# Optimization experiments

Measured on AMD Instinct MI355X. Metric: run time of the kernel, lower is better.

The kernel has to match this reference:

```python
import jax, jax.numpy as jnp
import numpy as np

H = 512      # hidden_dim
K = 3        # conv_kernel_size
CHUNK = 3    # chunk_size
EPS = 1e-5   # BatchNorm eps


def conv1d(x, w, b, pad):
    # x: (B, Cin, L), w: (Cout, Cin, K)
    y = jax.lax.conv_general_dilated(x, w, (1,), [(pad, pad)],
                                     dimension_numbers=("NCH", "OIH", "NCH"))
    return y + b[None, :, None]


def chunk_indices(seq_lens):
    # static int metadata -> numpy index build (loop over small fixed batch only)
    sl = np.asarray(seq_lens)
    bidx, sidx = [], []
    for b, l in enumerate(sl):
        starts = np.arange(0, int(l) - CHUNK + 1, CHUNK)
        bidx.append(np.full(starts.shape[0], b, dtype=np.int32))
        sidx.append(starts.astype(np.int32))
    return np.concatenate(bidx), np.concatenate(sidx)


def setup_inputs() -> dict:
    key = jax.random.key(0)
    ks = jax.random.split(key, 8)
    B, L = 32, 4096
    x = jax.random.normal(ks[0], (B, L), jnp.float32)
    seq_lens = jax.random.randint(ks[1], (B,), 2048, L + 1)

    def w(k, shape):
        return jax.random.normal(k, shape, jnp.float32) * 0.05

    return {
        "x": x,
        "w0": w(ks[2], (H, 1, K)), "b0": jnp.zeros((H,)), "g0": jnp.ones((H,)), "be0": jnp.zeros((H,)),
        "w1": w(ks[3], (H, H, K)), "b1": jnp.zeros((H,)), "g1": jnp.ones((H,)), "be1": jnp.zeros((H,)),
        "w2": w(ks[4], (H, H, K)), "b2": jnp.zeros((H,)), "g2": jnp.ones((H,)), "be2": jnp.zeros((H,)),
        "pw": w(ks[5], (H, H, CHUNK)), "pb": jnp.zeros((H,)),
        "fw": w(ks[6], (1, H)), "fb": jnp.zeros((1,)),
        "seq_lens": seq_lens,
    }


def reference(x, w0, b0, g0, be0, w1, b1, g1, be1, w2, b2, g2, be2,
              pw, pb, fw, fb, seq_lens):
    inv = np.float32(1.0 / np.sqrt(1.0 + EPS))  # BN eval: mean=0, var=1
    h = x[:, None, :]  # (B, 1, L)
    for (w, b, g, be) in ((w0, b0, g0, be0), (w1, b1, g1, be1), (w2, b2, g2, be2)):
        h = jax.nn.relu(conv1d(h, w, b, pad=1))
        h = (g * inv)[None, :, None] * h + be[None, :, None]
    h = jnp.transpose(h, (0, 2, 1))  # (B, L, H)

    bidx_np, sidx_np = chunk_indices(seq_lens)
    bidx = jnp.asarray(bidx_np)
    sidx = jnp.asarray(sidx_np)
    offs = jnp.arange(CHUNK, dtype=jnp.int32)
    chunks = h[bidx[:, None], sidx[:, None] + offs[None, :], :]  # (N, CHUNK, H)

    # pre_fc_conv over a length-CHUNK window == one GEMM per chunk
    z = jnp.einsum("nth,cht->nc", chunks, pw) + pb  # (N, H)
    logits = jax.nn.relu(z) @ fw.T + fb             # (N, 1)
    return jax.nn.sigmoid(logits)[:, 0]             # (N,)
```

## Files before the change

### kernel.cpp

```cpp
#include <hip/hip_runtime.h>

#define HCH 512
#define LSEQ 4096
#define NB 32
#define KW 3
#define KDIM 1536
#define SPAD 1408
#define INVS 0.9999950000374997f

typedef __attribute__((ext_vector_type(8))) short bf16x8;
typedef __attribute__((ext_vector_type(4))) float f32x4;

__device__ inline unsigned short f2bf(float f) {
  unsigned int u = __float_as_uint(f);
  u += 0x7fffu + ((u >> 16) & 1u);
  return (unsigned short)(u >> 16);
}

__device__ inline void gl_lds16(const void* g, void* l) {
  __builtin_amdgcn_global_load_lds(
      (const __attribute__((address_space(1))) void*)g,
      (__attribute__((address_space(3))) void*)l, 16, 0, 0);
}

__global__ void prepz(const int* __restrict__ seq_lens, int* __restrict__ cum,
                      float* __restrict__ p, int n) {
  int i = blockIdx.x * 256 + threadIdx.x;
  if (i < n) p[i] = 0.f;
  if (blockIdx.x == 0 && threadIdx.x == 0) {
    int acc = 0;
    for (int b = 0; b < NB; b++) {
      cum[b] = acc;
      acc += (seq_lens[b] - KW) / KW + 1;
    }
  }
}

__global__ void wtrans(const float* __restrict__ w1, const float* __restrict__ w2,
                       const float* __restrict__ pw, unsigned short* __restrict__ wt) {
  int idx = blockIdx.x * 256 + threadIdx.x;
  int which = idx / (HCH * KDIM);
  int r = idx % (HCH * KDIM);
  int c = r / KDIM;
  int rem = r % KDIM;
  int k = rem / HCH, ci = rem % HCH;
  const float* src = (which == 0) ? w1 : ((which == 1) ? w2 : pw);
  wt[idx] = f2bf(src[c * KDIM + ci * KW + k]);
}

__global__ void layer0(const float* __restrict__ x, const float* __restrict__ w0,
                       const float* __restrict__ b0, const float* __restrict__ g0,
                       const float* __restrict__ be0, unsigned short* __restrict__ h0) {
  int tid = threadIdx.x;
  int wave = tid >> 6, lane = tid & 63;
  int pos0 = (blockIdx.x * 4 + wave) * 8;
  int l0 = pos0 & (LSEQ - 1);
  int c0 = lane * 8;

  float w[24], bb[8], gg[8], ee[8];
  for (int v = 0; v < 6; v++)
    *reinterpret_cast<float4*>(w + v * 4) = *reinterpret_cast<const float4*>(w0 + c0 * 3 + v * 4);
  for (int v = 0; v < 2; v++) {
    *reinterpret_cast<float4*>(bb + v * 4) = *reinterpret_cast<const float4*>(b0 + c0 + v * 4);
    *reinterpret_cast<float4*>(gg + v * 4) = *reinterpret_cast<const float4*>(g0 + c0 + v * 4);
    *reinterpret_cast<float4*>(ee + v * 4) = *reinterpret_cast<const float4*>(be0 + c0 + v * 4);
  }
  for (int c = 0; c < 8; c++) gg[c] *= INVS;

  const float* xb = x + (size_t)(pos0 - l0);
  for (int pp = 0; pp < 8; pp++) {
    int l = l0 + pp;
    float xm1 = (l > 0) ? xb[l - 1] : 0.f;
    float xc = xb[l];
    float xp1 = (l < LSEQ - 1) ? xb[l + 1] : 0.f;
    unsigned int o[4];
    for (int pq = 0; pq < 4; pq++) {
      unsigned int lo = 0, hi = 0;
      for (int s = 0; s < 2; s++) {
        int c = pq * 2 + s;
        float y = w[c * 3] * xm1 + w[c * 3 + 1] * xc + w[c * 3 + 2] * xp1 + bb[c];
        y = fmaxf(y, 0.f);
        unsigned int u = f2bf(gg[c] * y + ee[c]);
        if (s == 0) lo = u; else hi = u;
      }
      o[pq] = lo | (hi << 16);
    }
    uint4 v4; v4.x = o[0]; v4.y = o[1]; v4.z = o[2]; v4.w = o[3];
    *reinterpret_cast<uint4*>(h0 + (size_t)(pos0 + pp) * HCH + c0) = v4;
  }
}

__global__ __launch_bounds__(256, 2) void conv_gemm(
    const unsigned short* __restrict__ hin,
    const unsigned short* __restrict__ wT,
    const float* __restrict__ bconv, const float* __restrict__ g,
    const float* __restrict__ be,
    unsigned short* __restrict__ hout,
    const unsigned short* __restrict__ zp) {
  __shared__ unsigned short As[3 * 128 * 32];
  __shared__ unsigned short Bs[272 * 32];

  int tid = threadIdx.x;
  int wave = tid >> 6, lane = tid & 63;
  int cm = blockIdx.x * 128;
  int ntile = blockIdx.y;
  int b = ntile >> 4;
  int l0 = (ntile & 15) << 8;
  int wn = wave * 64;
  const size_t hb = (size_t)b * LSEQ * HCH;

  f32x4 acc[8][4] = {};

  int lr = lane >> 2;
  int lc = (lane & 3) * 8;

  const unsigned short* bptr[4];
  for (int t = 0; t < 4; t++) {
    int p = l0 - 1 + (wave * 4 + t) * 16 + lr;
    bptr[t] = (p >= 0 && p < LSEQ) ? (hin + hb + (size_t)p * HCH + lc) : (zp + lc);
  }
  const unsigned short* hptr = zp + lc;
  if (wave == 3 && lane < 8) {
    int p = l0 + 255 + lr;
    hptr = (p < LSEQ) ? (hin + hb + (size_t)p * HCH + lc) : (zp + lc);
  }

  const unsigned short* aptr[6];
  unsigned aoff[6];
  for (int t = 0; t < 6; t++) {
    int s = wave * 6 + t;
    int k = s >> 3, c8 = s & 7;
    aptr[t] = wT + (size_t)(cm + c8 * 16 + lr) * KDIM + k * HCH + lc;
    aoff[t] = (unsigned)(k * 4096 + c8 * 512) * 2;
  }

  for (int it = 0; it < 16; it++) {
    int ci0 = it * 32;
    for (int t = 0; t < 6; t++)
      gl_lds16(aptr[t] + ci0, (char*)As + aoff[t]);
    for (int t = 0; t < 4; t++)
      gl_lds16(bptr[t] + ci0, (char*)Bs + (wave * 4 + t) * 1024);
    if (wave == 3)
      gl_lds16(hptr + ci0, (char*)Bs + 256 * 64);
    __syncthreads();

    int quad = lane >> 4, mr = lane & 15;
    for (int k = 0; k < 3; k++) {
      bf16x8 af[8], bfr[4];
      for (int i = 0; i < 8; i++)
        af[i] = *reinterpret_cast<const bf16x8*>(As + k * 4096 + (i * 16 + mr) * 32 + quad * 8);
      for (int j = 0; j < 4; j++)
        bfr[j] = *reinterpret_cast<const bf16x8*>(Bs + (wn + j * 16 + mr + k) * 32 + quad * 8);
      for (int i = 0; i < 8; i++)
        for (int j = 0; j < 4; j++)
          acc[i][j] = __builtin_amdgcn_mfma_f32_16x16x32_bf16(af[i], bfr[j], acc[i][j], 0, 0, 0);
    }
    __syncthreads();
  }

  int quad = lane >> 4, nn = lane & 15;
  for (int i = 0; i < 8; i++) {
    int c = cm + i * 16 + quad * 4;
    f32x4 bc = *reinterpret_cast<const f32x4*>(bconv + c);
    f32x4 gg = *reinterpret_cast<const f32x4*>(g + c);
    f32x4 bb = *reinterpret_cast<const f32x4*>(be + c);
    for (int j = 0; j < 4; j++) {
      int n = l0 + wn + j * 16 + nn;
      unsigned long long pack = 0;
      for (int r = 0; r < 4; r++) {
        float y = acc[i][j][r] + bc[r];
        y = fmaxf(y, 0.f);
        unsigned long long u = f2bf(gg[r] * INVS * y + bb[r]);
        pack |= u << (16 * r);
      }
      *reinterpret_cast<unsigned long long*>(hout + hb + (size_t)n * HCH + c) = pack;
    }
  }
}

__global__ __launch_bounds__(256) void chunk_gemm(
    const unsigned short* __restrict__ h2,
    const unsigned short* __restrict__ wTp,
    const float* __restrict__ pb, const float* __restrict__ fw,
    const int* __restrict__ seq_q,
    const int* __restrict__ cum_q,
    float* __restrict__ partial,
    const unsigned short* __restrict__ zp) {
  __shared__ unsigned short As[3 * 128 * 32];
  __shared__ unsigned short Bs[384 * 32];

  int tid = threadIdx.x;
  int wave = tid >> 6, lane = tid & 63;
  int cm = blockIdx.x * 128;
  int b = blockIdx.y / (SPAD / 128);
  int s_base = (blockIdx.y % (SPAD / 128)) * 128;
  int p_base = 3 * s_base;
  int slen = seq_q[b];
  int wm = (wave >> 1) * 64;
  int wn = (wave & 1) * 64;
  const size_t hb = (size_t)b * LSEQ * HCH;

  f32x4 acc[4][4] = {};

  int lr = lane >> 2, lc = (lane & 3) * 8;

  const unsigned short* bptr[6];
  const unsigned short* aptr[6];
  unsigned aoff[6];
  for (int t = 0; t < 6; t++) {
    int c = wave * 6 + t;
    int p = p_base + c * 16 + lr;
    bptr[t] = (p < LSEQ) ? (h2 + hb + (size_t)p * HCH + lc) : (zp + lc);
    int k = c >> 3, c8 = c & 7;
    aptr[t] = wTp + (size_t)(cm + c8 * 16 + lr) * KDIM + k * HCH + lc;
    aoff[t] = (unsigned)(k * 4096 + c8 * 512) * 2;
  }

  for (int it = 0; it < 16; it++) {
    int ci0 = it * 32;
    for (int t = 0; t < 6; t++) {
      gl_lds16(aptr[t] + ci0, (char*)As + aoff[t]);
      gl_lds16(bptr[t] + ci0, (char*)Bs + (wave * 6 + t) * 1024);
    }
    __syncthreads();

    int quad = lane >> 4, mr = lane & 15;
    for (int t = 0; t < 3; t++) {
      bf16x8 af[4], bfr[4];
      for (int i = 0; i < 4; i++)
        af[i] = *reinterpret_cast<const bf16x8*>(As + t * 4096 + (wm + i * 16 + mr) * 32 + quad * 8);
      for (int j = 0; j < 4; j++)
        bfr[j] = *reinterpret_cast<const bf16x8*>(Bs + (3 * (wn + j * 16 + mr) + t) * 32 + quad * 8);
      for (int i = 0; i < 4; i++)
        for (int j = 0; j < 4; j++)
          acc[i][j] = __builtin_amdgcn_mfma_f32_16x16x32_bf16(af[i], bfr[j], acc[i][j], 0, 0, 0);
    }
    __syncthreads();
  }

  int quad = lane >> 4, nn = lane & 15;
  for (int j = 0; j < 4; j++) {
    float s = 0.f;
    for (int i = 0; i < 4; i++) {
      int c = cm + wm + i * 16 + quad * 4;
      f32x4 pbv = *reinterpret_cast<const f32x4*>(pb + c);
      f32x4 fwv = *reinterpret_cast<const f32x4*>(fw + c);
      for (int r = 0; r < 4; r++) {
        float z = acc[i][j][r] + pbv[r];
        z = fmaxf(z, 0.f);
        s += z * fwv[r];
      }
    }
    s += __shfl_xor(s, 16, 64);
    s += __shfl_xor(s, 32, 64);
    if (quad == 0) {
      int sc = s_base + wn + j * 16 + nn;
      if (3 * sc + KW <= slen) atomicAdd(partial + cum_q[b] + sc, s);
    }
  }
}

__global__ void finalize(const float* __restrict__ partial, const float* __restrict__ fb,
                         float* __restrict__ out, int n) {
  int i = blockIdx.x * 256 + threadIdx.x;
  if (i < n) {
    float t = partial[i] + fb[0];
    out[i] = 1.f / (1.f + expf(-t));
  }
}

extern "C" void kernel_launch(void* const* d_in, const int* in_sizes, int n_in,
                              void* d_out, int out_size, void* d_ws, size_t ws_size,
                              hipStream_t stream) {
  (void)in_sizes; (void)n_in;
  const float* x   = (const float*)d_in[0];
  const float* w0  = (const float*)d_in[1];
  const float* b0  = (const float*)d_in[2];
  const float* g0  = (const float*)d_in[3];
  const float* be0 = (const float*)d_in[4];
  const float* w1  = (const float*)d_in[5];
  const float* b1  = (const float*)d_in[6];
  const float* g1  = (const float*)d_in[7];
  const float* be1 = (const float*)d_in[8];
  const float* w2  = (const float*)d_in[9];
  const float* b2  = (const float*)d_in[10];
  const float* g2  = (const float*)d_in[11];
  const float* be2 = (const float*)d_in[12];
  const float* pw  = (const float*)d_in[13];
  const float* pb  = (const float*)d_in[14];
  const float* fw  = (const float*)d_in[15];
  const float* fb  = (const float*)d_in[16];
  const int* seq_lens = (const int*)d_in[17];

  char* ws = (char*)d_ws;
  unsigned short* zeropage = (unsigned short*)ws;
  float* partial = (float*)(ws + 4096);
  size_t off = 4096 + (size_t)out_size * 4;
  off = (off + 255) & ~(size_t)255;
  int* cum = (int*)(ws + off);
  off += NB * 4;
  off = (off + 255) & ~(size_t)255;
  unsigned short* wt = (unsigned short*)(ws + off);
  off += (size_t)3 * HCH * KDIM * 2;
  off = (off + 255) & ~(size_t)255;
  size_t fixed = off;

  const size_t per_batch = (size_t)LSEQ * HCH * 2;
  int nb_pass = NB;
  while (nb_pass > 1 && fixed + 2 * per_batch * (size_t)nb_pass > ws_size)
    nb_pass >>= 1;
  unsigned short* h0 = (unsigned short*)(ws + fixed);
  unsigned short* h1 = h0 + (size_t)nb_pass * LSEQ * HCH;

  int nzero = 1024 + out_size;
  prepz<<<(nzero + 255) / 256, 256, 0, stream>>>(seq_lens, cum, (float*)ws, nzero);
  wtrans<<<(3 * HCH * KDIM) / 256, 256, 0, stream>>>(w1, w2, pw, wt);

  int npass = NB / nb_pass;
  for (int q = 0; q < npass; q++) {
    const float* xq = x + (size_t)q * nb_pass * LSEQ;
    layer0<<<nb_pass * (LSEQ / 32), 256, 0, stream>>>(xq, w0, b0, g0, be0, h0);
    conv_gemm<<<dim3(4, nb_pass * 16), 256, 0, stream>>>(h0, wt, b1, g1, be1, h1, zeropage);
    conv_gemm<<<dim3(4, nb_pass * 16), 256, 0, stream>>>(h1, wt + (size_t)HCH * KDIM,
                                                         b2, g2, be2, h0, zeropage);
    chunk_gemm<<<dim3(4, nb_pass * (SPAD / 128)), 256, 0, stream>>>(
        h0, wt + (size_t)2 * HCH * KDIM, pb, fw,
        seq_lens + q * nb_pass, cum + q * nb_pass, partial, zeropage);
  }
  finalize<<<(out_size + 255) / 256, 256, 0, stream>>>(partial, fb, (float*)d_out, out_size);
}
```

Baseline: 673.5 us.

## Load conv weights directly from global into registers and merge prep kernels

The conv_gemm kernel stops staging the weight tile (A operand) through LDS and instead has each lane read its bf16x8 weight fragments straight from global memory (L2/L1) inside the k loop, which removes the As buffer and its async copies. The two setup kernels (zeroing/cumulative counts and weight transpose) are merged into one launch to save a kernel launch. The trade-off is that each wave now issues its own global weight loads that are no longer shared through LDS across waves, and these loads sit on the MFMA critical path with higher latency. Less LDS use may allow higher occupancy.

```diff
diff --git a/kernel.cpp b/kernel.cpp
--- a/kernel.cpp
+++ b/kernel.cpp
@@ -23,29 +23,28 @@
       (__attribute__((address_space(3))) void*)l, 16, 0, 0);
 }
 
-__global__ void prepz(const int* __restrict__ seq_lens, int* __restrict__ cum,
-                      float* __restrict__ p, int n) {
-  int i = blockIdx.x * 256 + threadIdx.x;
-  if (i < n) p[i] = 0.f;
-  if (blockIdx.x == 0 && threadIdx.x == 0) {
+__global__ void prep_all(const float* __restrict__ w1, const float* __restrict__ w2,
+                         const float* __restrict__ pw, unsigned short* __restrict__ wt,
+                         const int* __restrict__ seq_lens, int* __restrict__ cum,
+                         float* __restrict__ pz, int nz) {
+  int idx = blockIdx.x * 256 + threadIdx.x;
+  if (idx < nz) pz[idx] = 0.f;
+  if (idx == 0) {
     int acc = 0;
     for (int b = 0; b < NB; b++) {
       cum[b] = acc;
       acc += (seq_lens[b] - KW) / KW + 1;
     }
   }
-}
-
-__global__ void wtrans(const float* __restrict__ w1, const float* __restrict__ w2,
-                       const float* __restrict__ pw, unsigned short* __restrict__ wt) {
-  int idx = blockIdx.x * 256 + threadIdx.x;
-  int which = idx / (HCH * KDIM);
-  int r = idx % (HCH * KDIM);
-  int c = r / KDIM;
-  int rem = r % KDIM;
-  int k = rem / HCH, ci = rem % HCH;
-  const float* src = (which == 0) ? w1 : ((which == 1) ? w2 : pw);
-  wt[idx] = f2bf(src[c * KDIM + ci * KW + k]);
+  if (idx < 3 * HCH * KDIM) {
+    int which = idx / (HCH * KDIM);
+    int r = idx % (HCH * KDIM);
+    int c = r / KDIM;
+    int rem = r % KDIM;
+    int k = rem / HCH, ci = rem % HCH;
+    const float* src = (which == 0) ? w1 : ((which == 1) ? w2 : pw);
+    wt[idx] = f2bf(src[c * KDIM + ci * KW + k]);
+  }
 }
 
 __global__ void layer0(const float* __restrict__ x, const float* __restrict__ w0,
@@ -97,7 +96,6 @@
     const float* __restrict__ be,
     unsigned short* __restrict__ hout,
     const unsigned short* __restrict__ zp) {
-  __shared__ unsigned short As[3 * 128 * 32];
   __shared__ unsigned short Bs[272 * 32];
 
   int tid = threadIdx.x;
@@ -125,30 +123,24 @@
     hptr = (p < LSEQ) ? (hin + hb + (size_t)p * HCH + lc) : (zp + lc);
   }
 
-  const unsigned short* aptr[6];
-  unsigned aoff[6];
-  for (int t = 0; t < 6; t++) {
-    int s = wave * 6 + t;
-    int k = s >> 3, c8 = s & 7;
-    aptr[t] = wT + (size_t)(cm + c8 * 16 + lr) * KDIM + k * HCH + lc;
-    aoff[t] = (unsigned)(k * 4096 + c8 * 512) * 2;
-  }
+  int quad = lane >> 4, mr = lane & 15;
+  const unsigned short* wTb = wT + (size_t)cm * KDIM;
+  unsigned vofA[8];
+  for (int i = 0; i < 8; i++)
+    vofA[i] = (unsigned)((i * 16 + mr) * KDIM + quad * 8);
 
   for (int it = 0; it < 16; it++) {
     int ci0 = it * 32;
-    for (int t = 0; t < 6; t++)
-      gl_lds16(aptr[t] + ci0, (char*)As + aoff[t]);
     for (int t = 0; t < 4; t++)
       gl_lds16(bptr[t] + ci0, (char*)Bs + (wave * 4 + t) * 1024);
     if (wave == 3)
       gl_lds16(hptr + ci0, (char*)Bs + 256 * 64);
     __syncthreads();
 
-    int quad = lane >> 4, mr = lane & 15;
     for (int k = 0; k < 3; k++) {
       bf16x8 af[8], bfr[4];
       for (int i = 0; i < 8; i++)
-        af[i] = *reinterpret_cast<const bf16x8*>(As + k * 4096 + (i * 16 + mr) * 32 + quad * 8);
+        af[i] = *reinterpret_cast<const bf16x8*>(wTb + vofA[i] + k * HCH + ci0);
       for (int j = 0; j < 4; j++)
         bfr[j] = *reinterpret_cast<const bf16x8*>(Bs + (wn + j * 16 + mr + k) * 32 + quad * 8);
       for (int i = 0; i < 8; i++)
@@ -158,7 +150,7 @@
     __syncthreads();
   }
 
-  int quad = lane >> 4, nn = lane & 15;
+  int nn = lane & 15;
   for (int i = 0; i < 8; i++) {
     int c = cm + i * 16 + quad * 4;
     f32x4 bc = *reinterpret_cast<const f32x4*>(bconv + c);
@@ -313,8 +305,8 @@
   unsigned short* h1 = h0 + (size_t)nb_pass * LSEQ * HCH;
 
   int nzero = 1024 + out_size;
-  prepz<<<(nzero + 255) / 256, 256, 0, stream>>>(seq_lens, cum, (float*)ws, nzero);
-  wtrans<<<(3 * HCH * KDIM) / 256, 256, 0, stream>>>(w1, w2, pw, wt);
+  prep_all<<<(3 * HCH * KDIM) / 256, 256, 0, stream>>>(w1, w2, pw, wt, seq_lens, cum,
+                                                       (float*)ws, nzero);
 
   int npass = NB / nb_pass;
   for (int q = 0; q < npass; q++) {
```

Result: slower. 1.097 ms (+62.9%).
